# Kernel tuning notes

Hardware: AMD Instinct MI355X
Metric: run time of the kernel (lower is better)

The kernel has to match this reference:

```python
import jax, jax.numpy as jnp
from jax import lax
import numpy as np

B, S, D, H = 16, 4096, 256, 256


def setup_inputs() -> dict:
    key = jax.random.key(0)
    k1, k2, k3, k4 = jax.random.split(key, 4)
    scale_x = 1.0 / np.sqrt(D)
    scale_h = 1.0 / np.sqrt(H)
    return {
        "inputs": jax.random.normal(k1, (B, S, D), dtype=jnp.float32),
        "state0": jnp.zeros((B, H), dtype=jnp.float32),
        "Wx": jax.random.normal(k2, (D, H), dtype=jnp.float32) * scale_x,
        "Wh": jax.random.normal(k3, (H, H), dtype=jnp.float32) * scale_h,
        "b": jnp.zeros((H,), dtype=jnp.float32),
    }


def reference(inputs, state0, Wx, Wh, b):
    # inputs: [B, S, D] -> time-major [S, B, D] (mirrors inputs.transpose_(0,1))
    x_tm = jnp.transpose(inputs, (1, 0, 2))
    # Precompute the input projection for all timesteps in one GEMM
    x_proj = jnp.einsum("sbd,dh->sbh", x_tm, Wx) + b  # [S, B, H]

    def step(h, xp_t):
        h_new = jnp.tanh(xp_t + h @ Wh)  # cell update; get_output = identity
        return h_new, h_new  # dropout p=0.0 -> identity

    _, outs = lax.scan(step, state0, x_proj)  # outs: [S, B, H]
    return jnp.transpose(outs, (1, 0, 2))  # back to [B, S, H]
```

## Files before the change

kernel.cpp:

```cpp
#include <hip/hip_runtime.h>

#define B_ 16
#define S_ 4096
#define D_ 256
#define H_ 256

typedef _Float16 h8v __attribute__((ext_vector_type(8)));
typedef float f4 __attribute__((ext_vector_type(4)));

static __device__ __forceinline__ void lds_barrier() {
    asm volatile("s_waitcnt lgkmcnt(0)" ::: "memory");
    __builtin_amdgcn_s_barrier();
}

__global__ __launch_bounds__(256) void xproj_kernel(
    const float* __restrict__ x, const float* __restrict__ Wx,
    const float* __restrict__ bias, float* __restrict__ out)
{
    __shared__ float xs[32 * 256];
    const int tid = threadIdx.x;
    const long long row0 = (long long)blockIdx.x * 32;

    {
        const f4* __restrict__ xg = (const f4*)(x + row0 * D_);
        f4* xsv = (f4*)xs;
        #pragma unroll
        for (int k = 0; k < 8; ++k)
            xsv[tid + k * 256] = xg[tid + k * 256];
    }
    __syncthreads();

    const int j = tid;
    float acc[32];
    const float bj = bias[j];
    #pragma unroll
    for (int r = 0; r < 32; ++r) acc[r] = bj;

    for (int d4 = 0; d4 < D_ / 4; ++d4) {
        const float w0 = Wx[(d4 * 4 + 0) * H_ + j];
        const float w1 = Wx[(d4 * 4 + 1) * H_ + j];
        const float w2 = Wx[(d4 * 4 + 2) * H_ + j];
        const float w3 = Wx[(d4 * 4 + 3) * H_ + j];
        #pragma unroll
        for (int r = 0; r < 32; ++r) {
            f4 xv = *(const f4*)&xs[r * 256 + d4 * 4];
            acc[r] = fmaf(xv.x, w0, acc[r]);
            acc[r] = fmaf(xv.y, w1, acc[r]);
            acc[r] = fmaf(xv.z, w2, acc[r]);
            acc[r] = fmaf(xv.w, w3, acc[r]);
        }
    }
    #pragma unroll
    for (int r = 0; r < 32; ++r)
        out[(row0 + r) * H_ + j] = acc[r];
}

__global__ __launch_bounds__(256, 1) void scan_kernel(
    const float* __restrict__ Wh, const float* __restrict__ state0,
    float* __restrict__ out)
{
    __shared__ __align__(16) _Float16 h_lds[2][H_];
    const int tid = threadIdx.x;
    const int l   = tid & 63;
    const int wav = tid >> 6;
    const int lc  = l & 15;
    const int kg  = l >> 4;
    const int b   = blockIdx.x;
    const int j_own = 64 * wav + 16 * kg + lc;

    h8v bf[4][8];
    #pragma unroll
    for (int nt = 0; nt < 4; ++nt) {
        const int j = 64 * wav + 16 * nt + lc;
        #pragma unroll
        for (int ks = 0; ks < 8; ++ks) {
            #pragma unroll
            for (int e = 0; e < 8; ++e) {
                const int k = 32 * ks + 8 * kg + e;
                bf[nt][ks][e] = (_Float16)Wh[k * H_ + j];
            }
        }
    }

    h_lds[0][tid] = (_Float16)state0[b * H_ + tid];

    float* __restrict__ outb = out + (long long)b * S_ * H_;

    float xr[4];
    #pragma unroll
    for (int k = 0; k < 4; ++k)
        xr[k] = outb[(long long)k * H_ + j_own];
    __syncthreads();

    const int abase = 8 * kg;

    #pragma unroll 4
    for (int st = 0; st < S_; ++st) {
        const int p = st & 1;
        const _Float16* hb = h_lds[p];

        h8v af[8];
        #pragma unroll
        for (int ks = 0; ks < 8; ++ks)
            af[ks] = *(const h8v*)&hb[32 * ks + abase];

        f4 acc0 = {0.f, 0.f, 0.f, 0.f};
        f4 acc1 = {0.f, 0.f, 0.f, 0.f};
        f4 acc2 = {0.f, 0.f, 0.f, 0.f};
        f4 acc3 = {0.f, 0.f, 0.f, 0.f};
        #pragma unroll
        for (int ks = 0; ks < 8; ++ks) {
            acc0 = __builtin_amdgcn_mfma_f32_16x16x32_f16(af[ks], bf[0][ks], acc0, 0, 0, 0);
            acc1 = __builtin_amdgcn_mfma_f32_16x16x32_f16(af[ks], bf[1][ks], acc1, 0, 0, 0);
            acc2 = __builtin_amdgcn_mfma_f32_16x16x32_f16(af[ks], bf[2][ks], acc2, 0, 0, 0);
            acc3 = __builtin_amdgcn_mfma_f32_16x16x32_f16(af[ks], bf[3][ks], acc3, 0, 0, 0);
        }

        float v = acc0[0];
        v = (kg == 1) ? acc1[0] : v;
        v = (kg == 2) ? acc2[0] : v;
        v = (kg == 3) ? acc3[0] : v;

        const float pre = v + xr[st & 3];
        const float e = __builtin_amdgcn_exp2f(pre * 2.8853900817779268f);
        const float hn = fmaf(-2.f, __builtin_amdgcn_rcpf(e + 1.f), 1.f);

        outb[(long long)st * H_ + j_own] = hn;
        h_lds[p ^ 1][j_own] = (_Float16)hn;

        const int nt4 = st + 4;
        xr[st & 3] = (nt4 < S_) ? outb[(long long)nt4 * H_ + j_own] : 0.f;
        lds_barrier();
    }
}

extern "C" void kernel_launch(void* const* d_in, const int* in_sizes, int n_in,
                              void* d_out, int out_size, void* d_ws, size_t ws_size,
                              hipStream_t stream) {
    const float* x  = (const float*)d_in[0];
    const float* s0 = (const float*)d_in[1];
    const float* Wx = (const float*)d_in[2];
    const float* Wh = (const float*)d_in[3];
    const float* bv = (const float*)d_in[4];
    float* out = (float*)d_out;

    xproj_kernel<<<dim3((B_ * S_) / 32), dim3(256), 0, stream>>>(x, Wx, bv, out);
    scan_kernel<<<dim3(B_), dim3(256), 0, stream>>>(Wh, s0, out);
}
```

Before: 1.919 ms.

## Split recurrent matvec between MFMA and VALU dot2 with DPP reductions

Each wave now computes half of its 64 hidden columns with MFMA (2 tiles instead of 4). The other half uses packed fp16 dot2 instructions on the VALU, with partial sums reduced across lanes through DPP moves. The goal is to shorten the per-step critical path of the serial scan by running the matrix and vector units in parallel. The cost is more register pressure, extra LDS reads, predicated ownership of outputs, and a smaller unroll factor.

```diff
diff --git a/kernel.cpp b/kernel.cpp
--- a/kernel.cpp
+++ b/kernel.cpp
@@ -5,8 +5,22 @@
 #define D_ 256
 #define H_ 256
 
+typedef _Float16 h2 __attribute__((ext_vector_type(2)));
 typedef _Float16 h8v __attribute__((ext_vector_type(8)));
 typedef float f4 __attribute__((ext_vector_type(4)));
+
+static __device__ __forceinline__ float fdot2f(h2 a, h2 b, float c) {
+    return __builtin_amdgcn_fdot2(a, b, c, false);
+}
+
+template <int CTRL>
+static __device__ __forceinline__ float dpp_mv(float v) {
+    int r = __builtin_amdgcn_update_dpp(0, __float_as_int(v), CTRL, 0xF, 0xF, true);
+    return __int_as_float(r);
+}
+#define DPP_XOR1  0xB1
+#define DPP_XOR2  0x4E
+#define DPP_HMIRR 0x141
 
 static __device__ __forceinline__ void lds_barrier() {
     asm volatile("s_waitcnt lgkmcnt(0)" ::: "memory");
@@ -65,12 +79,13 @@
     const int wav = tid >> 6;
     const int lc  = l & 15;
     const int kg  = l >> 4;
+    const int g3  = l >> 3;
+    const int sl3 = l & 7;
     const int b   = blockIdx.x;
-    const int j_own = 64 * wav + 16 * kg + lc;
-
-    h8v bf[4][8];
-    #pragma unroll
-    for (int nt = 0; nt < 4; ++nt) {
+
+    h8v bf[2][8];
+    #pragma unroll
+    for (int nt = 0; nt < 2; ++nt) {
         const int j = 64 * wav + 16 * nt + lc;
         #pragma unroll
         for (int ks = 0; ks < 8; ++ks) {
@@ -81,24 +96,53 @@
             }
         }
     }
+    const int j_m = 64 * wav + 16 * kg + lc;
+    const bool own_m = (kg < 2);
+
+    const bool b2v = (sl3 & 4) != 0;
+    const bool b1v = (sl3 & 2) != 0;
+    const int jv_own = 64 * wav + 32 + 4 * g3 + (b2v ? 2 : 0) + (b1v ? 1 : 0);
+    const bool own_v = (sl3 & 1) == 0;
+    h2 wv[4][16];
+    #pragma unroll
+    for (int jj = 0; jj < 4; ++jj) {
+        const int jv = 64 * wav + 32 + 4 * g3 + jj;
+        #pragma unroll
+        for (int p = 0; p < 16; ++p) {
+            const int k = 32 * sl3 + 2 * p;
+            h2 q;
+            q[0] = (_Float16)Wh[(long long)k * H_ + jv];
+            q[1] = (_Float16)Wh[(long long)(k + 1) * H_ + jv];
+            wv[jj][p] = q;
+        }
+    }
 
     h_lds[0][tid] = (_Float16)state0[b * H_ + tid];
 
     float* __restrict__ outb = out + (long long)b * S_ * H_;
 
-    float xr[4];
-    #pragma unroll
-    for (int k = 0; k < 4; ++k)
-        xr[k] = outb[(long long)k * H_ + j_own];
+    float xrM[4], xrV[4];
+    #pragma unroll
+    for (int k = 0; k < 4; ++k) {
+        xrM[k] = outb[(long long)k * H_ + j_m];
+        xrV[k] = outb[(long long)k * H_ + jv_own];
+    }
     __syncthreads();
 
     const int abase = 8 * kg;
-
-    #pragma unroll 4
+    const int vbase = 32 * sl3;
+
+    #pragma unroll 2
     for (int st = 0; st < S_; ++st) {
         const int p = st & 1;
         const _Float16* hb = h_lds[p];
 
+        union { h8v v; h2 q[4]; } u0, u1, u2, u3;
+        u0.v = *(const h8v*)&hb[vbase];
+        u1.v = *(const h8v*)&hb[vbase + 8];
+        u2.v = *(const h8v*)&hb[vbase + 16];
+        u3.v = *(const h8v*)&hb[vbase + 24];
+
         h8v af[8];
         #pragma unroll
         for (int ks = 0; ks < 8; ++ks)
@@ -106,30 +150,72 @@
 
         f4 acc0 = {0.f, 0.f, 0.f, 0.f};
         f4 acc1 = {0.f, 0.f, 0.f, 0.f};
-        f4 acc2 = {0.f, 0.f, 0.f, 0.f};
-        f4 acc3 = {0.f, 0.f, 0.f, 0.f};
         #pragma unroll
         for (int ks = 0; ks < 8; ++ks) {
             acc0 = __builtin_amdgcn_mfma_f32_16x16x32_f16(af[ks], bf[0][ks], acc0, 0, 0, 0);
             acc1 = __builtin_amdgcn_mfma_f32_16x16x32_f16(af[ks], bf[1][ks], acc1, 0, 0, 0);
-            acc2 = __builtin_amdgcn_mfma_f32_16x16x32_f16(af[ks], bf[2][ks], acc2, 0, 0, 0);
-            acc3 = __builtin_amdgcn_mfma_f32_16x16x32_f16(af[ks], bf[3][ks], acc3, 0, 0, 0);
-        }
-
-        float v = acc0[0];
-        v = (kg == 1) ? acc1[0] : v;
-        v = (kg == 2) ? acc2[0] : v;
-        v = (kg == 3) ? acc3[0] : v;
-
-        const float pre = v + xr[st & 3];
-        const float e = __builtin_amdgcn_exp2f(pre * 2.8853900817779268f);
-        const float hn = fmaf(-2.f, __builtin_amdgcn_rcpf(e + 1.f), 1.f);
-
-        outb[(long long)st * H_ + j_own] = hn;
-        h_lds[p ^ 1][j_own] = (_Float16)hn;
+        }
+
+        float a0 = 0.f, a1 = 0.f, a2 = 0.f, a3 = 0.f;
+        #pragma unroll
+        for (int m = 0; m < 4; ++m) {
+            a0 = fdot2f(u0.q[m], wv[0][m], a0);
+            a1 = fdot2f(u0.q[m], wv[1][m], a1);
+            a2 = fdot2f(u0.q[m], wv[2][m], a2);
+            a3 = fdot2f(u0.q[m], wv[3][m], a3);
+        }
+        #pragma unroll
+        for (int m = 0; m < 4; ++m) {
+            a0 = fdot2f(u1.q[m], wv[0][4 + m], a0);
+            a1 = fdot2f(u1.q[m], wv[1][4 + m], a1);
+            a2 = fdot2f(u1.q[m], wv[2][4 + m], a2);
+            a3 = fdot2f(u1.q[m], wv[3][4 + m], a3);
+        }
+        #pragma unroll
+        for (int m = 0; m < 4; ++m) {
+            a0 = fdot2f(u2.q[m], wv[0][8 + m], a0);
+            a1 = fdot2f(u2.q[m], wv[1][8 + m], a1);
+            a2 = fdot2f(u2.q[m], wv[2][8 + m], a2);
+            a3 = fdot2f(u2.q[m], wv[3][8 + m], a3);
+        }
+        #pragma unroll
+        for (int m = 0; m < 4; ++m) {
+            a0 = fdot2f(u3.q[m], wv[0][12 + m], a0);
+            a1 = fdot2f(u3.q[m], wv[1][12 + m], a1);
+            a2 = fdot2f(u3.q[m], wv[2][12 + m], a2);
+            a3 = fdot2f(u3.q[m], wv[3][12 + m], a3);
+        }
+
+        float kA = b2v ? a2 : a0, sA = b2v ? a0 : a2;
+        float kB = b2v ? a3 : a1, sB = b2v ? a1 : a3;
+        kA += dpp_mv<DPP_HMIRR>(sA);
+        kB += dpp_mv<DPP_HMIRR>(sB);
+        float nn = b1v ? kB : kA, snd = b1v ? kA : kB;
+        nn += dpp_mv<DPP_XOR2>(snd);
+        nn += dpp_mv<DPP_XOR1>(nn);
+
+        const float vm = (kg == 1) ? acc1[0] : acc0[0];
+        const float preM = vm + xrM[st & 3];
+        const float preV = nn + xrV[st & 3];
+        const float eM = __builtin_amdgcn_exp2f(preM * 2.8853900817779268f);
+        const float eV = __builtin_amdgcn_exp2f(preV * 2.8853900817779268f);
+        const float hnM = fmaf(-2.f, __builtin_amdgcn_rcpf(eM + 1.f), 1.f);
+        const float hnV = fmaf(-2.f, __builtin_amdgcn_rcpf(eV + 1.f), 1.f);
+
+        if (own_m) {
+            outb[(long long)st * H_ + j_m] = hnM;
+            h_lds[p ^ 1][j_m] = (_Float16)hnM;
+        }
+        if (own_v) {
+            outb[(long long)st * H_ + jv_own] = hnV;
+            h_lds[p ^ 1][jv_own] = (_Float16)hnV;
+        }
 
         const int nt4 = st + 4;
-        xr[st & 3] = (nt4 < S_) ? outb[(long long)nt4 * H_ + j_own] : 0.f;
+        if (nt4 < S_) {
+            xrM[st & 3] = outb[(long long)nt4 * H_ + j_m];
+            xrV[st & 3] = outb[(long long)nt4 * H_ + jv_own];
+        }
         lds_barrier();
     }
 }
```

After: 4.032 ms. 2.1x slower.
